# Kernel optimization log

Hardware: AMD Instinct MI355X
Metric: run time of the kernel (lower is better)

The kernel has to match this reference:

```python
import jax, jax.numpy as jnp
import numpy as np

N_NODES = 50000
N_EDGES = 800000
D = 128


def setup_inputs() -> dict:
    key = jax.random.key(0)
    ks = jax.random.split(key, 8)
    h = jax.random.normal(ks[0], (N_NODES, D), dtype=jnp.float32)
    src = jax.random.randint(ks[1], (N_EDGES,), 0, N_NODES, dtype=jnp.int64)
    dst = jax.random.randint(ks[2], (N_EDGES,), 0, N_NODES, dtype=jnp.int64)
    # Glorot-ish init for the three GraphConv weights
    scale = 1.0 / np.sqrt(D)
    W0 = jax.random.normal(ks[3], (D, D), dtype=jnp.float32) * scale
    W1 = jax.random.normal(ks[4], (D, D), dtype=jnp.float32) * scale
    W2 = jax.random.normal(ks[5], (D, D), dtype=jnp.float32) * scale
    b0 = jnp.zeros((D,), dtype=jnp.float32)
    b1 = jnp.zeros((D,), dtype=jnp.float32)
    b2 = jnp.zeros((D,), dtype=jnp.float32)
    return {"h": h, "src": src, "dst": dst, "W0": W0, "b0": b0,
            "W1": W1, "b1": b1, "W2": W2, "b2": b2}


def _graph_conv(x, src, dst, W, b, n_nodes):
    """DGL GraphConv, norm='both', activation=ReLU.
    in_feats == out_feats -> aggregate first, then matmul W."""
    ones = jnp.ones_like(src, dtype=x.dtype)
    out_deg = jnp.clip(jax.ops.segment_sum(ones, src, num_segments=n_nodes), 1.0)
    in_deg = jnp.clip(jax.ops.segment_sum(ones, dst, num_segments=n_nodes), 1.0)
    x = x * (out_deg ** -0.5)[:, None]          # src-side normalization
    m = jax.ops.segment_sum(x[src], dst, num_segments=n_nodes)  # sparse aggregation
    m = m * (in_deg ** -0.5)[:, None]           # dst-side normalization
    return jax.nn.relu(m @ W + b)


def reference(h, src, dst, W0, b0, W1, b1, W2, b2):
    n = h.shape[0]
    h = _graph_conv(h, src, dst, W0, b0, n)
    h = _graph_conv(h, src, dst, W1, b1, n)
    h = _graph_conv(h, src, dst, W2, b2, n)
    return h
```

## Files before the change

kernel.cpp:

```cpp
#include <hip/hip_runtime.h>

#define N_NODES 50000
#define N_EDGES 800000
#define D 128
#define CAP 48
#define MS_STRIDE 132

typedef __attribute__((ext_vector_type(4))) float f32x4;
typedef __attribute__((ext_vector_type(8))) short s16x8;

__device__ inline unsigned short f32_to_bf16_rtne(float f) {
    union { float f; unsigned u; } c; c.f = f;
    unsigned u = c.u;
    u += 0x7FFF + ((u >> 16) & 1);
    return (unsigned short)(u >> 16);
}
__device__ inline float bf16_to_f32(unsigned short h) {
    union { unsigned u; float f; } c; c.u = ((unsigned)h) << 16;
    return c.f;
}
__device__ inline unsigned pack_bf2(float a, float b) {
    return (unsigned)f32_to_bf16_rtne(a) | ((unsigned)f32_to_bf16_rtne(b) << 16);
}
__device__ inline void unpack_bf2(unsigned u, float& a, float& b) {
    union { unsigned u; float f; } c0, c1;
    c0.u = u << 16; c1.u = u & 0xFFFF0000u;
    a = c0.f; b = c1.f;
}
__device__ inline void acc_uint4(uint4 v, float* a) {
    float f0, f1;
    unpack_bf2(v.x, f0, f1); a[0] += f0; a[1] += f1;
    unpack_bf2(v.y, f0, f1); a[2] += f0; a[3] += f1;
    unpack_bf2(v.z, f0, f1); a[4] += f0; a[5] += f1;
    unpack_bf2(v.w, f0, f1); a[6] += f0; a[7] += f1;
}


__global__ __launch_bounds__(256) void fill_slots(const int* __restrict__ src,
                                                  const int* __restrict__ dst,
                                                  int* __restrict__ cursor,
                                                  int* __restrict__ cnt_out,
                                                  int* __restrict__ slots) {
    int e = blockIdx.x * 256 + threadIdx.x;
    if (e < N_EDGES) {
        int d = dst[e], s = src[e];
        int p = atomicAdd(&cursor[d], 1);
        if (p < CAP) slots[d * CAP + p] = s;
        atomicAdd(&cnt_out[s], 1);
    }
}

__global__ __launch_bounds__(256) void norms(const int* __restrict__ cursor,
                                             const int* __restrict__ cnt_out,
                                             float* __restrict__ s_in,
                                             float* __restrict__ s_out) {
    int i = blockIdx.x * 256 + threadIdx.x;
    if (i < N_NODES) {
        s_in[i]  = rsqrtf(fmaxf((float)cursor[i], 1.0f));
        s_out[i] = rsqrtf(fmaxf((float)cnt_out[i], 1.0f));
    }
}


__global__ __launch_bounds__(256) void hconv(const float4* __restrict__ h,
                                             const float* __restrict__ s_out,
                                             uint2* __restrict__ hb) {
    int gid = blockIdx.x * 256 + threadIdx.x;
    if (gid >= N_NODES * 32) return;
    float so = s_out[gid >> 5];
    float4 v = h[gid];
    hb[gid] = make_uint2(pack_bf2(so * v.x, so * v.y), pack_bf2(so * v.z, so * v.w));
}


__global__ __launch_bounds__(256) void pack_w(const float* __restrict__ W0,
                                              const float* __restrict__ W1,
                                              const float* __restrict__ W2,
                                              s16x8* __restrict__ wpk) {
    int tid = threadIdx.x;
    int wid = blockIdx.x * 4 + (tid >> 6);
    if (wid >= 96) return;
    int lane = tid & 63;
    int layer = wid / 32, rem = wid % 32;
    int ct = rem >> 2, ks = rem & 3;
    const float* W = (layer == 0) ? W0 : (layer == 1) ? W1 : W2;
    int col = ct * 16 + (lane & 15);
    int k0  = ks * 32 + (lane >> 4) * 8;
    s16x8 hi, lo;
#pragma unroll
    for (int j = 0; j < 8; j++) {
        float w = W[(k0 + j) * D + col];
        unsigned short h = f32_to_bf16_rtne(w);
        hi[j] = (short)h;
        lo[j] = (short)f32_to_bf16_rtne(w - bf16_to_f32(h));
    }
    int idx = layer * 4096 + (ct * 4 + ks) * 64 + lane;
    wpk[idx]        = hi;
    wpk[idx + 2048] = lo;
}


__global__ __launch_bounds__(256) void fused_layer(const uint4* __restrict__ x,
                                                   const int* __restrict__ slots,
                                                   const int* __restrict__ deg,
                                                   const float* __restrict__ s_in,
                                                   const s16x8* __restrict__ wpk,
                                                   const float* __restrict__ bias,
                                                   const float* __restrict__ s_out,
                                                   float* __restrict__ outf,
                                                   unsigned short* __restrict__ outb) {
    __shared__ float mS[16 * MS_STRIDE];
    int tid = threadIdx.x;
    int row0 = blockIdx.x * 16;

    {
        int nloc = tid >> 4;
        int l    = tid & 15;
        int node = row0 + nloc;
        int dg = min(deg[node], CAP);
        int base = node * CAP;
        float a[8];
#pragma unroll
        for (int j = 0; j < 8; j++) a[j] = 0.f;
        int e = 0;
        for (; e + 4 <= dg; e += 4) {
            int s0 = slots[base + e],     s1 = slots[base + e + 1];
            int s2 = slots[base + e + 2], s3 = slots[base + e + 3];
            uint4 v0 = x[s0 * 16 + l];
            uint4 v1 = x[s1 * 16 + l];
            uint4 v2 = x[s2 * 16 + l];
            uint4 v3 = x[s3 * 16 + l];
            acc_uint4(v0, a); acc_uint4(v1, a); acc_uint4(v2, a); acc_uint4(v3, a);
        }
        for (; e < dg; e++) {
            uint4 v0 = x[slots[base + e] * 16 + l];
            acc_uint4(v0, a);
        }
        float si = s_in[node];
        float* dp = &mS[nloc * MS_STRIDE + l * 8];
#pragma unroll
        for (int j = 0; j < 8; j++) dp[j] = a[j] * si;
    }
    __syncthreads();

    int wv = tid >> 6;
    int lane = tid & 63;
    int arow = lane & 15, aq = lane >> 4;
    int ct0 = wv * 2, ct1 = ct0 + 1;
    f32x4 acc0 = (f32x4)0.f, acc1 = (f32x4)0.f;

#pragma unroll
    for (int ks = 0; ks < 4; ks++) {
        const float* ap = &mS[arow * MS_STRIDE + ks * 32 + aq * 8];
        s16x8 ahi, alo;
#pragma unroll
        for (int j = 0; j < 8; j++) {
            float av = ap[j];
            unsigned short hh = f32_to_bf16_rtne(av);
            ahi[j] = (short)hh;
            alo[j] = (short)f32_to_bf16_rtne(av - bf16_to_f32(hh));
        }
        int idx0 = (ct0 * 4 + ks) * 64 + lane;
        int idx1 = (ct1 * 4 + ks) * 64 + lane;
        s16x8 b0h = wpk[idx0], b0l = wpk[idx0 + 2048];
        s16x8 b1h = wpk[idx1], b1l = wpk[idx1 + 2048];
        acc0 = __builtin_amdgcn_mfma_f32_16x16x32_bf16(ahi, b0h, acc0, 0, 0, 0);
        acc0 = __builtin_amdgcn_mfma_f32_16x16x32_bf16(alo, b0h, acc0, 0, 0, 0);
        acc0 = __builtin_amdgcn_mfma_f32_16x16x32_bf16(ahi, b0l, acc0, 0, 0, 0);
        acc1 = __builtin_amdgcn_mfma_f32_16x16x32_bf16(ahi, b1h, acc1, 0, 0, 0);
        acc1 = __builtin_amdgcn_mfma_f32_16x16x32_bf16(alo, b1h, acc1, 0, 0, 0);
        acc1 = __builtin_amdgcn_mfma_f32_16x16x32_bf16(ahi, b1l, acc1, 0, 0, 0);
    }

    int crow0 = aq * 4;
    float so4[4];
    if (outb) {
#pragma unroll
        for (int r = 0; r < 4; r++) so4[r] = s_out[row0 + crow0 + r];
    }
    int colA = ct0 * 16 + arow, colB = ct1 * 16 + arow;
    float bA = bias[colA], bB = bias[colB];
#pragma unroll
    for (int r = 0; r < 4; r++) {
        size_t rowoff = (size_t)(row0 + crow0 + r) * D;
        float vA = fmaxf(acc0[r] + bA, 0.f);
        float vB = fmaxf(acc1[r] + bB, 0.f);
        if (outf) { outf[rowoff + colA] = vA; outf[rowoff + colB] = vB; }
        if (outb) {
            outb[rowoff + colA] = f32_to_bf16_rtne(so4[r] * vA);
            outb[rowoff + colB] = f32_to_bf16_rtne(so4[r] * vB);
        }
    }
}


extern "C" void kernel_launch(void* const* d_in, const int* in_sizes, int n_in,
                              void* d_out, int out_size, void* d_ws, size_t ws_size,
                              hipStream_t stream) {
    const float* h  = (const float*)d_in[0];
    const int*  src = (const int*)d_in[1];
    const int*  dst = (const int*)d_in[2];
    const float* W0 = (const float*)d_in[3];
    const float* b0 = (const float*)d_in[4];
    const float* W1 = (const float*)d_in[5];
    const float* b1 = (const float*)d_in[6];
    const float* W2 = (const float*)d_in[7];
    const float* b2 = (const float*)d_in[8];
    float* out = (float*)d_out;

    char* w = (char*)d_ws;
    auto carve = [&](size_t bytes) -> void* {
        void* p = (void*)w;
        w += (bytes + 255) & ~(size_t)255;
        return p;
    };
    int*   cnt     = (int*)carve(2 * N_NODES * sizeof(int));
    int*   cursor  = cnt;
    int*   cnt_out = cnt + N_NODES;
    float* s_in    = (float*)carve(N_NODES * sizeof(float));
    float* s_out   = (float*)carve(N_NODES * sizeof(float));
    int*   slots   = (int*)carve((size_t)N_NODES * CAP * sizeof(int));
    unsigned short* actA = (unsigned short*)carve((size_t)N_NODES * D * 2);
    unsigned short* actB = (unsigned short*)carve((size_t)N_NODES * D * 2);
    s16x8* wpk     = (s16x8*)carve(3 * 4096 * sizeof(s16x8));

    hipMemsetAsync(cnt, 0, 2 * N_NODES * sizeof(int), stream);
    fill_slots<<<(N_EDGES + 255) / 256, 256, 0, stream>>>(src, dst, cursor, cnt_out, slots);
    norms<<<(N_NODES + 255) / 256, 256, 0, stream>>>(cursor, cnt_out, s_in, s_out);
    hconv<<<(N_NODES * 32 + 255) / 256, 256, 0, stream>>>((const float4*)h, s_out, (uint2*)actA);
    pack_w<<<24, 256, 0, stream>>>(W0, W1, W2, wpk);

    const int GRID = N_NODES / 16;

    fused_layer<<<GRID, 256, 0, stream>>>((const uint4*)actA, slots, cursor, s_in,
                                          wpk, b0, s_out, nullptr, actB);
    fused_layer<<<GRID, 256, 0, stream>>>((const uint4*)actB, slots, cursor, s_in,
                                          wpk + 4096, b1, s_out, nullptr, actA);
    fused_layer<<<GRID, 256, 0, stream>>>((const uint4*)actA, slots, cursor, s_in,
                                          wpk + 8192, b2, s_out, out, nullptr);
}
```

Measured before the change: 291.5 us.

## Batch neighbor gathers with shuffled indices and LDS histogram for out-degree

The aggregation loop now loads up to 48 neighbor indices cooperatively across 16 lanes, broadcasts them with shuffles, and double-buffers groups of 8 row gathers so more loads are in flight. Padded slots point to an extra zero row appended to each activation buffer, which removes the tail branch. Out-degree counting moves from global atomics to per-block shared-memory byte-packed histograms plus a reduction, and the norms kernel is fused into the bf16 conversion kernel. The byte-packed counters assume fewer than 256 hits per node per block, and the padded gathers read the zero row even for low-degree nodes.

Result: faster. 279.5 us (-4.1%).

```diff
diff --git a/kernel.cpp b/kernel.cpp
--- a/kernel.cpp
+++ b/kernel.cpp
@@ -5,6 +5,9 @@
 #define D 128
 #define CAP 48
 #define MS_STRIDE 132
+#define HISTB 256
+#define EPB (N_EDGES / HISTB)
+#define HWORDS (N_NODES / 4)
 
 typedef __attribute__((ext_vector_type(4))) float f32x4;
 typedef __attribute__((ext_vector_type(8))) short s16x8;
@@ -35,41 +38,88 @@
     unpack_bf2(v.w, f0, f1); a[6] += f0; a[7] += f1;
 }
 
+struct R8 { uint4 g0, g1, g2, g3, g4, g5, g6, g7; };
+
+__device__ inline void load8(R8& G, const uint4* __restrict__ x, int v, int k, int l) {
+    G.g0 = x[__shfl(v, k + 0, 16) * 16 + l];
+    G.g1 = x[__shfl(v, k + 1, 16) * 16 + l];
+    G.g2 = x[__shfl(v, k + 2, 16) * 16 + l];
+    G.g3 = x[__shfl(v, k + 3, 16) * 16 + l];
+    G.g4 = x[__shfl(v, k + 4, 16) * 16 + l];
+    G.g5 = x[__shfl(v, k + 5, 16) * 16 + l];
+    G.g6 = x[__shfl(v, k + 6, 16) * 16 + l];
+    G.g7 = x[__shfl(v, k + 7, 16) * 16 + l];
+}
+__device__ inline void acc8(const R8& G, float* a) {
+    acc_uint4(G.g0, a); acc_uint4(G.g1, a); acc_uint4(G.g2, a); acc_uint4(G.g3, a);
+    acc_uint4(G.g4, a); acc_uint4(G.g5, a); acc_uint4(G.g6, a); acc_uint4(G.g7, a);
+}
+
+
+__global__ __launch_bounds__(256) void hist_src(const int* __restrict__ src,
+                                                unsigned* __restrict__ partial) {
+    __shared__ unsigned hist[HWORDS];
+    for (int i = threadIdx.x; i < HWORDS; i += 256) hist[i] = 0;
+    __syncthreads();
+    int e0 = blockIdx.x * EPB;
+    for (int i = threadIdx.x; i < EPB; i += 256) {
+        int s = src[e0 + i];
+        atomicAdd(&hist[s >> 2], 1u << ((s & 3) * 8));
+    }
+    __syncthreads();
+    unsigned* dst = partial + (size_t)blockIdx.x * HWORDS;
+    for (int i = threadIdx.x; i < HWORDS; i += 256) dst[i] = hist[i];
+}
+
+__global__ __launch_bounds__(256) void reduce_hist(const unsigned* __restrict__ partial,
+                                                   int* __restrict__ cnt_out) {
+    int w = blockIdx.x * 256 + threadIdx.x;
+    if (w >= HWORDS) return;
+    int c0 = 0, c1 = 0, c2 = 0, c3 = 0;
+    for (int b = 0; b < HISTB; b++) {
+        unsigned v = partial[(size_t)b * HWORDS + w];
+        c0 += v & 255; c1 += (v >> 8) & 255; c2 += (v >> 16) & 255; c3 += v >> 24;
+    }
+    ((int4*)cnt_out)[w] = make_int4(c0, c1, c2, c3);
+}
+
 
 __global__ __launch_bounds__(256) void fill_slots(const int* __restrict__ src,
                                                   const int* __restrict__ dst,
                                                   int* __restrict__ cursor,
-                                                  int* __restrict__ cnt_out,
                                                   int* __restrict__ slots) {
     int e = blockIdx.x * 256 + threadIdx.x;
     if (e < N_EDGES) {
         int d = dst[e], s = src[e];
         int p = atomicAdd(&cursor[d], 1);
         if (p < CAP) slots[d * CAP + p] = s;
-        atomicAdd(&cnt_out[s], 1);
-    }
-}
-
-__global__ __launch_bounds__(256) void norms(const int* __restrict__ cursor,
-                                             const int* __restrict__ cnt_out,
-                                             float* __restrict__ s_in,
-                                             float* __restrict__ s_out) {
-    int i = blockIdx.x * 256 + threadIdx.x;
-    if (i < N_NODES) {
-        s_in[i]  = rsqrtf(fmaxf((float)cursor[i], 1.0f));
-        s_out[i] = rsqrtf(fmaxf((float)cnt_out[i], 1.0f));
-    }
-}
-
-
-__global__ __launch_bounds__(256) void hconv(const float4* __restrict__ h,
-                                             const float* __restrict__ s_out,
-                                             uint2* __restrict__ hb) {
+    }
+}
+
+
+__global__ __launch_bounds__(256) void hconv_norms(const float4* __restrict__ h,
+                                                   const int* __restrict__ cursor,
+                                                   const int* __restrict__ cnt_out,
+                                                   float* __restrict__ s_in,
+                                                   float* __restrict__ s_out,
+                                                   uint2* __restrict__ hbA,
+                                                   uint2* __restrict__ hbB) {
     int gid = blockIdx.x * 256 + threadIdx.x;
-    if (gid >= N_NODES * 32) return;
-    float so = s_out[gid >> 5];
-    float4 v = h[gid];
-    hb[gid] = make_uint2(pack_bf2(so * v.x, so * v.y), pack_bf2(so * v.z, so * v.w));
+    const int total = N_NODES * 32;
+    if (gid < total) {
+        int node = gid >> 5;
+        float so = rsqrtf(fmaxf((float)cnt_out[node], 1.0f));
+        if ((gid & 31) == 0) {
+            s_out[node] = so;
+            s_in[node]  = rsqrtf(fmaxf((float)cursor[node], 1.0f));
+        }
+        float4 v = h[gid];
+        hbA[gid] = make_uint2(pack_bf2(so * v.x, so * v.y), pack_bf2(so * v.z, so * v.w));
+    } else if (gid < total + 32) {
+        hbA[total + (gid - total)] = make_uint2(0u, 0u);
+    } else if (gid < total + 64) {
+        hbB[total + (gid - total - 32)] = make_uint2(0u, 0u);
+    }
 }
 
 
@@ -119,22 +169,34 @@
         int node = row0 + nloc;
         int dg = min(deg[node], CAP);
         int base = node * CAP;
+        int idx0 = (l      < dg) ? slots[base + l]      : N_NODES;
+        int idx1 = (16 + l < dg) ? slots[base + 16 + l] : N_NODES;
+        int idx2 = (32 + l < dg) ? slots[base + 32 + l] : N_NODES;
+
         float a[8];
 #pragma unroll
         for (int j = 0; j < 8; j++) a[j] = 0.f;
-        int e = 0;
-        for (; e + 4 <= dg; e += 4) {
-            int s0 = slots[base + e],     s1 = slots[base + e + 1];
-            int s2 = slots[base + e + 2], s3 = slots[base + e + 3];
-            uint4 v0 = x[s0 * 16 + l];
-            uint4 v1 = x[s1 * 16 + l];
-            uint4 v2 = x[s2 * 16 + l];
-            uint4 v3 = x[s3 * 16 + l];
-            acc_uint4(v0, a); acc_uint4(v1, a); acc_uint4(v2, a); acc_uint4(v3, a);
-        }
-        for (; e < dg; e++) {
-            uint4 v0 = x[slots[base + e] * 16 + l];
-            acc_uint4(v0, a);
+
+        int nr = (dg + 7) >> 3;
+        if (nr > 0) {
+            R8 A, B;
+            auto chunk = [&](int r) { int c = r >> 1; return c == 0 ? idx0 : (c == 1 ? idx1 : idx2); };
+            load8(A, x, chunk(0), 0, l);
+            int r = 1;
+            while (r + 1 < nr) {
+                load8(B, x, chunk(r), (r & 1) * 8, l);
+                acc8(A, a);
+                load8(A, x, chunk(r + 1), ((r + 1) & 1) * 8, l);
+                acc8(B, a);
+                r += 2;
+            }
+            if (r < nr) {
+                load8(B, x, chunk(r), (r & 1) * 8, l);
+                acc8(A, a);
+                acc8(B, a);
+            } else {
+                acc8(A, a);
+            }
         }
         float si = s_in[node];
         float* dp = &mS[nloc * MS_STRIDE + l * 8];
@@ -214,20 +276,22 @@
         w += (bytes + 255) & ~(size_t)255;
         return p;
     };
-    int*   cnt     = (int*)carve(2 * N_NODES * sizeof(int));
-    int*   cursor  = cnt;
-    int*   cnt_out = cnt + N_NODES;
-    float* s_in    = (float*)carve(N_NODES * sizeof(float));
-    float* s_out   = (float*)carve(N_NODES * sizeof(float));
-    int*   slots   = (int*)carve((size_t)N_NODES * CAP * sizeof(int));
-    unsigned short* actA = (unsigned short*)carve((size_t)N_NODES * D * 2);
-    unsigned short* actB = (unsigned short*)carve((size_t)N_NODES * D * 2);
-    s16x8* wpk     = (s16x8*)carve(3 * 4096 * sizeof(s16x8));
-
-    hipMemsetAsync(cnt, 0, 2 * N_NODES * sizeof(int), stream);
-    fill_slots<<<(N_EDGES + 255) / 256, 256, 0, stream>>>(src, dst, cursor, cnt_out, slots);
-    norms<<<(N_NODES + 255) / 256, 256, 0, stream>>>(cursor, cnt_out, s_in, s_out);
-    hconv<<<(N_NODES * 32 + 255) / 256, 256, 0, stream>>>((const float4*)h, s_out, (uint2*)actA);
+    int*      cursor  = (int*)carve(N_NODES * sizeof(int));
+    int*      cnt_out = (int*)carve(N_NODES * sizeof(int));
+    float*    s_in    = (float*)carve(N_NODES * sizeof(float));
+    float*    s_out   = (float*)carve(N_NODES * sizeof(float));
+    int*      slots   = (int*)carve((size_t)N_NODES * CAP * sizeof(int));
+    unsigned* partial = (unsigned*)carve((size_t)HISTB * HWORDS * sizeof(unsigned));
+    unsigned short* actA = (unsigned short*)carve((size_t)(N_NODES + 1) * D * 2);
+    unsigned short* actB = (unsigned short*)carve((size_t)(N_NODES + 1) * D * 2);
+    s16x8*    wpk     = (s16x8*)carve(3 * 4096 * sizeof(s16x8));
+
+    hipMemsetAsync(cursor, 0, N_NODES * sizeof(int), stream);
+    hist_src<<<HISTB, 256, 0, stream>>>(src, partial);
+    reduce_hist<<<(HWORDS + 255) / 256, 256, 0, stream>>>(partial, cnt_out);
+    fill_slots<<<(N_EDGES + 255) / 256, 256, 0, stream>>>(src, dst, cursor, slots);
+    hconv_norms<<<(N_NODES * 32 + 64 + 255) / 256, 256, 0, stream>>>((const float4*)h, cursor, cnt_out,
+                                                                     s_in, s_out, (uint2*)actA, (uint2*)actB);
     pack_w<<<24, 256, 0, stream>>>(W0, W1, W2, wpk);
 
     const int GRID = N_NODES / 16;
```
